# Optimization experiments

Hardware: AMD Instinct MI355X
Metric: run time of the kernel (lower is better)

Reference implementation:

```python
import jax, jax.numpy as jnp
import numpy as np

B, S, D = 1, 2048, 2048
H, KV, HD = 16, 8, 128
FF = 6144
EPS = 1e-6
THETA = 1e6
PRUNE_K = int(0.3 * S)  # tokens evicted this layer


def _rms(x, w):
    v = jnp.mean(jnp.square(x), axis=-1, keepdims=True)
    return x * jax.lax.rsqrt(v + EPS) * w


def _rope(x, cos, sin):
    # x: [B, h, S, HD]; rotate_half convention (Qwen/LLaMA style)
    x1, x2 = jnp.split(x, 2, axis=-1)
    rot = jnp.concatenate([-x2, x1], axis=-1)
    return x * cos + rot * sin


def setup_inputs() -> dict:
    key = jax.random.key(0)
    ks = jax.random.split(key, 8)
    sc = 0.02
    causal = jnp.where(jnp.tril(jnp.ones((S, S), bool)), 0.0, -1e9).astype(jnp.float32)
    return {
        "hidden_states": jax.random.normal(ks[0], (B, S, D), jnp.float32),
        "causal_mask": causal[None, None],  # [1,1,S,S]
        "positions": jnp.arange(S, dtype=jnp.int32),
        "in_ln_w": jnp.ones((D,), jnp.float32),
        "post_ln_w": jnp.ones((D,), jnp.float32),
        "q_norm_w": jnp.ones((HD,), jnp.float32),
        "k_norm_w": jnp.ones((HD,), jnp.float32),
        "Wq": jax.random.normal(ks[1], (D, H * HD), jnp.float32) * sc,
        "Wk": jax.random.normal(ks[2], (D, KV * HD), jnp.float32) * sc,
        "Wv": jax.random.normal(ks[3], (D, KV * HD), jnp.float32) * sc,
        "Wo": jax.random.normal(ks[4], (H * HD, D), jnp.float32) * sc,
        "W_gate": jax.random.normal(ks[5], (D, FF), jnp.float32) * sc,
        "W_up": jax.random.normal(ks[6], (D, FF), jnp.float32) * sc,
        "W_down": jax.random.normal(ks[7], (FF, D), jnp.float32) * sc,
    }


def reference(hidden_states, causal_mask, positions, in_ln_w, post_ln_w,
              q_norm_w, k_norm_w, Wq, Wk, Wv, Wo, W_gate, W_up, W_down):
    # Rotary tables (Qwen3 rope_theta)
    inv = 1.0 / (THETA ** (jnp.arange(0, HD, 2, dtype=jnp.float32) / HD))
    ang = positions.astype(jnp.float32)[:, None] * inv[None, :]      # [S, HD/2]
    cos = jnp.concatenate([jnp.cos(ang)] * 2, -1)[None, None]        # [1,1,S,HD]
    sin = jnp.concatenate([jnp.sin(ang)] * 2, -1)[None, None]

    # --- self attention block ---
    x = _rms(hidden_states, in_ln_w)
    q = (x @ Wq).reshape(B, S, H, HD).transpose(0, 2, 1, 3)
    k = (x @ Wk).reshape(B, S, KV, HD).transpose(0, 2, 1, 3)
    v = (x @ Wv).reshape(B, S, KV, HD).transpose(0, 2, 1, 3)
    q = _rope(_rms(q, q_norm_w), cos, sin)   # Qwen3 per-head QK-norm then RoPE
    k = _rope(_rms(k, k_norm_w), cos, sin)
    rep = H // KV
    k = jnp.repeat(k, rep, axis=1)
    v = jnp.repeat(v, rep, axis=1)
    scores = jnp.einsum('bhqd,bhkd->bhqk', q, k) / np.float32(np.sqrt(HD)) + causal_mask
    attn = jax.nn.softmax(scores, axis=-1)   # [B,H,S,S] (output_attentions=True)
    ctx = jnp.einsum('bhqk,bhkd->bhqd', attn, v)
    attn_out = ctx.transpose(0, 2, 1, 3).reshape(B, S, H * HD) @ Wo
    h = hidden_states + attn_out

    # --- MLP block (SwiGLU) ---
    y = _rms(h, post_ln_w)
    mlp = (jax.nn.silu(y @ W_gate) * (y @ W_up)) @ W_down
    out = h + mlp

    # --- importance scoring + top-k pruning (prefill: last token is index S-1) ---
    importance = jnp.sum(attn[:, :, S - 1, :], axis=(0, 1)) / (B * H)  # [S]
    importance = importance.at[S - 1].set(jnp.inf)  # never prune the last token
    _, prune_idxs = jax.lax.top_k(-importance, PRUNE_K)  # k smallest scores
    return out, attn, prune_idxs
```

## Files before the change

kernel.cpp:

```cpp
#include <hip/hip_runtime.h>
#include <math.h>

#define Sn 2048
#define Dm 2048
#define Hn 16
#define KVn 8
#define HD 128
#define FFn 6144
#define PK 614

#define BM 64
#define BN 64
#define BK 16

typedef __attribute__((ext_vector_type(8))) short short8;
typedef __attribute__((ext_vector_type(4))) float f32x4;

__device__ __forceinline__ short f2bf(float f) {
    unsigned u = __float_as_uint(f);
    u += 0x7fff + ((u >> 16) & 1);
    return (short)(u >> 16);
}

__device__ __forceinline__ void gload16(const void* g, void* l) {
    __builtin_amdgcn_global_load_lds((const __attribute__((address_space(1))) void*)g,
                                     (__attribute__((address_space(3))) void*)l, 16, 0, 0);
}

template<typename ACC, int MODE>
__global__ __launch_bounds__(256)
void gemm_k(const float* __restrict__ A, int lda, long long strideA,
            const float* __restrict__ B, int ldb, long long strideB, int bshift,
            float* __restrict__ C, int ldc, long long strideC,
            const float* __restrict__ resid,
            int M, int N, int K, float alpha, int causal)
{
    const int bx = blockIdx.x, by = blockIdx.y, bz = blockIdx.z;
    const int bm0 = by * BM, bn0 = bx * BN;
    if (MODE == 1 && causal == 1 && bn0 > bm0 + BM - 1) return;

    A += (long long)bz * strideA;
    B += (long long)(bz >> bshift) * strideB;
    C += (long long)bz * strideC;

    __shared__ float As[BK][BM + 4];
    __shared__ float Bs[BK][BN + 4];

    const int tid = threadIdx.x;
    const int tx = tid & 15, ty = tid >> 4;

    ACC acc[4][4];
    #pragma unroll
    for (int i = 0; i < 4; i++)
        #pragma unroll
        for (int j = 0; j < 4; j++) acc[i][j] = (ACC)0;

    for (int k0 = 0; k0 < K; k0 += BK) {
        {
            int c = tid & 15, r0 = tid >> 4;
            #pragma unroll
            for (int i = 0; i < 4; i++) {
                int r = r0 + 16 * i;
                As[c][r] = A[(long long)(bm0 + r) * lda + (k0 + c)];
            }
        }
        if (MODE == 1) {
            int c = tid & 15, r0 = tid >> 4;
            #pragma unroll
            for (int i = 0; i < 4; i++) {
                int r = r0 + 16 * i;
                Bs[c][r] = B[(long long)(bn0 + r) * ldb + (k0 + c)];
            }
        } else {
            int c = tid & 63, r0 = tid >> 6;
            #pragma unroll
            for (int i = 0; i < 4; i++) {
                int r = r0 + 4 * i;
                Bs[r][c] = B[(long long)(k0 + r) * ldb + (bn0 + c)];
            }
        }
        __syncthreads();
        #pragma unroll
        for (int kk = 0; kk < BK; kk++) {
            float4 av = *(const float4*)&As[kk][ty * 4];
            float4 bv = *(const float4*)&Bs[kk][tx * 4];
            float a_[4] = {av.x, av.y, av.z, av.w};
            float b_[4] = {bv.x, bv.y, bv.z, bv.w};
            #pragma unroll
            for (int i = 0; i < 4; i++)
                #pragma unroll
                for (int j = 0; j < 4; j++)
                    acc[i][j] += (ACC)a_[i] * (ACC)b_[j];
        }
        __syncthreads();
    }

    #pragma unroll
    for (int i = 0; i < 4; i++) {
        int m = bm0 + ty * 4 + i;
        #pragma unroll
        for (int j = 0; j < 4; j++) {
            int n = bn0 + tx * 4 + j;
            float val = (float)(acc[i][j] * (ACC)alpha);
            if (resid) val += resid[(long long)m * ldc + n];
            C[(long long)m * ldc + n] = val;
        }
    }
}

template<int MODE>
__global__ __launch_bounds__(256)
void mgemm_k(const short* __restrict__ A, int lda,
             const short* __restrict__ B, int ldb,
             const short* __restrict__ B2,
             float* __restrict__ Cf, short* __restrict__ Cb, int ldc,
             const float* __restrict__ resid, int K)
{
    __shared__ short As[128 * 64];
    __shared__ short Bs[128 * 64];
    __shared__ short B2s[(MODE == 1) ? 128 * 64 : 16];

    const int tid = threadIdx.x, lane = tid & 63, wv = tid >> 6;
    const int wm = wv & 1, wn = wv >> 1;
    const int l15 = lane & 15, q4 = lane >> 4;
    const int bm0 = blockIdx.y * 128, bn0 = blockIdx.x * 128;

    f32x4 acc[4][4];
    f32x4 acc2[(MODE == 1) ? 4 : 1][(MODE == 1) ? 4 : 1];
    #pragma unroll
    for (int i = 0; i < 4; i++)
        #pragma unroll
        for (int j = 0; j < 4; j++) {
            acc[i][j] = (f32x4)0.0f;
            if constexpr (MODE == 1) acc2[i][j] = (f32x4)0.0f;
        }

    for (int k0 = 0; k0 < K; k0 += 64) {
        #pragma unroll
        for (int r = 0; r < 4; r++) {
            int c = (wv * 4 + r) * 64 + lane;
            int row = c >> 3, co = (c & 7) * 8;
            gload16(A + (size_t)(bm0 + row) * lda + k0 + co, (char*)As + (size_t)c * 16);
            gload16(B + (size_t)(bn0 + row) * ldb + k0 + co, (char*)Bs + (size_t)c * 16);
            if constexpr (MODE == 1)
                gload16(B2 + (size_t)(bn0 + row) * ldb + k0 + co, (char*)B2s + (size_t)c * 16);
        }
        __syncthreads();
        #pragma unroll
        for (int kk = 0; kk < 2; kk++) {
            short8 af[4], bfr[4], b2f[4];
            #pragma unroll
            for (int i = 0; i < 4; i++)
                af[i] = *(const short8*)&As[(size_t)(wm * 64 + i * 16 + l15) * 64 + kk * 32 + q4 * 8];
            #pragma unroll
            for (int j = 0; j < 4; j++) {
                bfr[j] = *(const short8*)&Bs[(size_t)(wn * 64 + j * 16 + l15) * 64 + kk * 32 + q4 * 8];
                if constexpr (MODE == 1)
                    b2f[j] = *(const short8*)&B2s[(size_t)(wn * 64 + j * 16 + l15) * 64 + kk * 32 + q4 * 8];
            }
            #pragma unroll
            for (int i = 0; i < 4; i++)
                #pragma unroll
                for (int j = 0; j < 4; j++) {
                    acc[i][j] = __builtin_amdgcn_mfma_f32_16x16x32_bf16(af[i], bfr[j], acc[i][j], 0, 0, 0);
                    if constexpr (MODE == 1)
                        acc2[i][j] = __builtin_amdgcn_mfma_f32_16x16x32_bf16(af[i], b2f[j], acc2[i][j], 0, 0, 0);
                }
        }
        __syncthreads();
    }

    #pragma unroll
    for (int i = 0; i < 4; i++)
        #pragma unroll
        for (int j = 0; j < 4; j++)
            #pragma unroll
            for (int r = 0; r < 4; r++) {
                int m = bm0 + wm * 64 + i * 16 + q4 * 4 + r;
                int n = bn0 + wn * 64 + j * 16 + l15;
                float vv = acc[i][j][r];
                if constexpr (MODE == 0) {
                    if (resid) vv += resid[(size_t)m * ldc + n];
                    Cf[(size_t)m * ldc + n] = vv;
                } else if constexpr (MODE == 1) {
                    float u = acc2[i][j][r];
                    Cb[(size_t)m * ldc + n] = f2bf(vv / (1.0f + expf(-vv)) * u);
                } else {
                    Cb[(size_t)n * ldc + m] = f2bf(vv);
                }
            }
}

__global__ __launch_bounds__(256)
void ctx_k(const float* __restrict__ P, const short* __restrict__ Vt,
           short* __restrict__ Cb)
{
    __shared__ float Af[128 * 64];
    __shared__ short Bs[128 * 64];

    const int h = blockIdx.z;
    const float* A = P + (size_t)h * Sn * Sn;
    const short* B = Vt + (size_t)(h >> 1) * HD * Sn;

    const int tid = threadIdx.x, lane = tid & 63, wv = tid >> 6;
    const int wm = wv & 1, wn = wv >> 1;
    const int l15 = lane & 15, q4 = lane >> 4;
    const int bm0 = blockIdx.y * 128;
    const int Keff = bm0 + 128;

    f32x4 acc[4][4];
    #pragma unroll
    for (int i = 0; i < 4; i++)
        #pragma unroll
        for (int j = 0; j < 4; j++) acc[i][j] = (f32x4)0.0f;

    for (int k0 = 0; k0 < Keff; k0 += 64) {
        #pragma unroll
        for (int r = 0; r < 8; r++) {
            int c = (wv * 8 + r) * 64 + lane;
            int row = c >> 4, co = (c & 15) * 4;
            gload16(A + (size_t)(bm0 + row) * Sn + k0 + co, (char*)Af + (size_t)c * 16);
        }
        #pragma unroll
        for (int r = 0; r < 4; r++) {
            int c = (wv * 4 + r) * 64 + lane;
            int row = c >> 3, co = (c & 7) * 8;
            gload16(B + (size_t)row * Sn + k0 + co, (char*)Bs + (size_t)c * 16);
        }
        __syncthreads();
        #pragma unroll
        for (int kk = 0; kk < 2; kk++) {
            short8 af[4], bfr[4];
            #pragma unroll
            for (int i = 0; i < 4; i++) {
                const float* ap = &Af[(size_t)(wm * 64 + i * 16 + l15) * 64 + kk * 32 + q4 * 8];
                f32x4 a0 = *(const f32x4*)ap;
                f32x4 a1 = *(const f32x4*)(ap + 4);
                short8 t;
                t[0] = f2bf(a0[0]); t[1] = f2bf(a0[1]); t[2] = f2bf(a0[2]); t[3] = f2bf(a0[3]);
                t[4] = f2bf(a1[0]); t[5] = f2bf(a1[1]); t[6] = f2bf(a1[2]); t[7] = f2bf(a1[3]);
                af[i] = t;
            }
            #pragma unroll
            for (int j = 0; j < 4; j++)
                bfr[j] = *(const short8*)&Bs[(size_t)(wn * 64 + j * 16 + l15) * 64 + kk * 32 + q4 * 8];
            #pragma unroll
            for (int i = 0; i < 4; i++)
                #pragma unroll
                for (int j = 0; j < 4; j++)
                    acc[i][j] = __builtin_amdgcn_mfma_f32_16x16x32_bf16(af[i], bfr[j], acc[i][j], 0, 0, 0);
        }
        __syncthreads();
    }

    #pragma unroll
    for (int i = 0; i < 4; i++)
        #pragma unroll
        for (int j = 0; j < 4; j++)
            #pragma unroll
            for (int r = 0; r < 4; r++) {
                int m = bm0 + wm * 64 + i * 16 + q4 * 4 + r;
                int n = wn * 64 + j * 16 + l15;
                Cb[(size_t)m * Dm + h * HD + n] = f2bf(acc[i][j][r]);
            }
}

__global__ __launch_bounds__(256)
void castT_k(const float* __restrict__ W, int ldw, int row0, int col0,
             short* __restrict__ Wt, int ldt)
{
    __shared__ float t[64][65];
    const int tr = threadIdx.x >> 6, tc = threadIdx.x & 63;
    const int gr = blockIdx.y * 64, gc = blockIdx.x * 64;
    #pragma unroll
    for (int rr = tr; rr < 64; rr += 4)
        t[rr][tc] = W[(size_t)(row0 + gr + rr) * ldw + col0 + gc + tc];
    __syncthreads();
    #pragma unroll
    for (int cc = tr; cc < 64; cc += 4)
        Wt[(size_t)(gc + cc) * ldt + gr + tc] = f2bf(t[tc][cc]);
}

__global__ __launch_bounds__(256)
void rmsnorm_k(const float* __restrict__ in, const float* __restrict__ w,
               float* __restrict__ o, short* __restrict__ ob)
{
    const int row = blockIdx.x;
    const float* x = in + (long long)row * Dm;
    const int tid = threadIdx.x;
    double ss = 0.0;
    #pragma unroll
    for (int rb = 0; rb < 8; rb++) {
        float t = x[tid + rb * 256];
        ss += (double)t * (double)t;
    }
    #pragma unroll
    for (int off = 32; off > 0; off >>= 1) ss += __shfl_xor(ss, off, 64);
    __shared__ double sh[4];
    int lane = tid & 63, wvv = tid >> 6;
    if (lane == 0) sh[wvv] = ss;
    __syncthreads();
    double tot = sh[0] + sh[1] + sh[2] + sh[3];
    double scale = 1.0 / sqrt(tot / (double)Dm + (double)1e-6f);
    #pragma unroll
    for (int rb = 0; rb < 8; rb++) {
        int j = tid + rb * 256;
        float val = (float)((double)x[j] * scale * (double)w[j]);
        if (o)  o[(long long)row * Dm + j] = val;
        if (ob) ob[(long long)row * Dm + j] = f2bf(val);
    }
}

__global__ __launch_bounds__(256)
void rope_table_k(const int* __restrict__ positions,
                  double* __restrict__ ct, double* __restrict__ st)
{
    int idx = blockIdx.x * 256 + threadIdx.x;
    if (idx >= Sn * 64) return;
    int s = idx >> 6, j = idx & 63;
    float e = (float)j * (1.0f / 64.0f);
    float p32 = (float)pow(1.0e6, (double)e);
    float invf = (float)(1.0 / (double)p32);
    float ang = (float)positions[s] * invf;
    ct[idx] = cos((double)ang);
    st[idx] = sin((double)ang);
}

__global__ __launch_bounds__(128)
void qknorm_rope_k(float* __restrict__ buf, int ld, int nh,
                   const float* __restrict__ w,
                   const double* __restrict__ ct, const double* __restrict__ st)
{
    const int b = blockIdx.x;
    const int h = b % nh, s = b / nh;
    float* p = buf + (long long)s * ld + h * HD;
    const int d = threadIdx.x;
    const int pd = (d < 64) ? d + 64 : d - 64;
    float a = p[d];
    float pv = p[pd];
    double ss = (double)a * (double)a;
    #pragma unroll
    for (int o = 32; o > 0; o >>= 1) ss += __shfl_xor(ss, o, 64);
    __shared__ double sh[2];
    if ((d & 63) == 0) sh[d >> 6] = ss;
    __syncthreads();
    double tot = sh[0] + sh[1];
    double scale = 1.0 / sqrt(tot / (double)HD + (double)1e-6f);
    double xn = (double)a * scale * (double)w[d];
    double pn = (double)pv * scale * (double)w[pd];
    double rot = (d < 64) ? -pn : pn;
    int j = d & 63;
    double c = ct[s * 64 + j], snv = st[s * 64 + j];
    p[d] = (float)(xn * c + rot * snv);
}

__global__ __launch_bounds__(256)
void qlast_proj_k(const float* __restrict__ x, const float* __restrict__ Wq,
                  double* __restrict__ qlast)
{
    __shared__ double part[4][64];
    const int kq = threadIdx.x >> 6, nn = threadIdx.x & 63;
    const int n = blockIdx.x * 64 + nn;
    const float* xr = x + (size_t)(Sn - 1) * Dm;
    double acc = 0.0;
    for (int k = kq; k < Dm; k += 4)
        acc += (double)xr[k] * (double)Wq[(size_t)k * Dm + n];
    part[kq][nn] = acc;
    __syncthreads();
    if (kq == 0)
        qlast[n] = part[0][nn] + part[1][nn] + part[2][nn] + part[3][nn];
}

__global__ __launch_bounds__(128)
void qlast_nr_k(const double* __restrict__ qlast, const float* __restrict__ w,
                const double* __restrict__ ct, const double* __restrict__ st,
                double* __restrict__ qhat)
{
    const int h = blockIdx.x, d = threadIdx.x;
    const int pd = (d < 64) ? d + 64 : d - 64;
    double a = qlast[h * HD + d];
    double pv = qlast[h * HD + pd];
    double ss = a * a;
    #pragma unroll
    for (int o = 32; o > 0; o >>= 1) ss += __shfl_xor(ss, o, 64);
    __shared__ double sh[2];
    if ((d & 63) == 0) sh[d >> 6] = ss;
    __syncthreads();
    double tot = sh[0] + sh[1];
    double scale = 1.0 / sqrt(tot / (double)HD + (double)1e-6f);
    double xn = a * scale * (double)w[d];
    double pn = pv * scale * (double)w[pd];
    double rot = (d < 64) ? -pn : pn;
    int j = d & 63;
    double c = ct[(Sn - 1) * 64 + j], snv = st[(Sn - 1) * 64 + j];
    qhat[h * HD + d] = xn * c + rot * snv;
}

__global__ __launch_bounds__(256)
void imp_scores_k(const double* __restrict__ qhat, const float* __restrict__ khat,
                  double* __restrict__ phead)
{
    const int h = blockIdx.x, kv = h >> 1;
    __shared__ double sc[Sn];
    __shared__ double qv[HD];
    __shared__ double sh[4];
    const int tid = threadIdx.x;
    if (tid < HD) qv[tid] = qhat[h * HD + tid];
    __syncthreads();
    const double s128 = (double)sqrtf(128.0f);
    for (int j = tid; j < Sn; j += 256) {
        const float* kr = khat + (long long)j * (KVn * HD) + kv * HD;
        double acc = 0.0;
        #pragma unroll 8
        for (int dd = 0; dd < HD; dd++) acc += qv[dd] * (double)kr[dd];
        sc[j] = acc / s128;
    }
    __syncthreads();
    double m = -1.0e300;
    for (int j = tid; j < Sn; j += 256) m = fmax(m, sc[j]);
    #pragma unroll
    for (int o = 32; o > 0; o >>= 1) m = fmax(m, __shfl_xor(m, o, 64));
    if ((tid & 63) == 0) sh[tid >> 6] = m;
    __syncthreads();
    m = fmax(fmax(sh[0], sh[1]), fmax(sh[2], sh[3]));
    __syncthreads();
    double ssum = 0.0;
    for (int j = tid; j < Sn; j += 256) {
        double e = exp(sc[j] - m);
        sc[j] = e;
        ssum += e;
    }
    #pragma unroll
    for (int o = 32; o > 0; o >>= 1) ssum += __shfl_xor(ssum, o, 64);
    if ((tid & 63) == 0) sh[tid >> 6] = ssum;
    __syncthreads();
    double tot = sh[0] + sh[1] + sh[2] + sh[3];
    for (int j = tid; j < Sn; j += 256)
        phead[(long long)h * Sn + j] = sc[j] / tot;
}

__global__ __launch_bounds__(1024)
void imp_sort_k(const double* __restrict__ phead, float* __restrict__ out_idx)
{
    __shared__ unsigned long long keys[Sn];
    const int tid = threadIdx.x;
    for (int j = tid; j < Sn; j += 1024) {
        double s = 0.0;
        #pragma unroll
        for (int h = 0; h < Hn; h++) s += phead[(long long)h * Sn + j];
        float imp = (float)(s * (1.0 / 16.0));
        if (j == Sn - 1) imp = __builtin_inff();
        unsigned u = __float_as_uint(imp);
        keys[j] = ((unsigned long long)u << 32) | (unsigned)j;
    }
    __syncthreads();
    for (int k = 2; k <= Sn; k <<= 1) {
        for (int jj = k >> 1; jj > 0; jj >>= 1) {
            for (int i = tid; i < Sn; i += 1024) {
                int p = i ^ jj;
                if (p > i) {
                    unsigned long long a = keys[i], b = keys[p];
                    bool up = ((i & k) == 0);
                    if ((a > b) == up) { keys[i] = b; keys[p] = a; }
                }
            }
            __syncthreads();
        }
    }
    if (tid < PK)
        out_idx[tid] = (float)(unsigned)(keys[tid] & 0xffffffffULL);
}

__global__ __launch_bounds__(256)
void softmax_k(float* __restrict__ attn)
{
    const long long row = blockIdx.x;
    const int i = (int)(row & (Sn - 1));
    float* p = attn + row * Sn;
    const int tid = threadIdx.x;
    float v[8];
    float mx = -1e30f;
    #pragma unroll
    for (int rb = 0; rb < 8; rb++) {
        int j = tid + rb * 256;
        if (j <= i) { v[rb] = p[j]; mx = fmaxf(mx, v[rb]); }
        else        v[rb] = 0.0f;
    }
    #pragma unroll
    for (int o = 32; o > 0; o >>= 1) mx = fmaxf(mx, __shfl_xor(mx, o, 64));
    __shared__ float shm[4], shs[4];
    int lane = tid & 63, wvv = tid >> 6;
    if (lane == 0) shm[wvv] = mx;
    __syncthreads();
    mx = fmaxf(fmaxf(shm[0], shm[1]), fmaxf(shm[2], shm[3]));
    float sum = 0.0f;
    #pragma unroll
    for (int rb = 0; rb < 8; rb++) {
        int j = tid + rb * 256;
        if (j <= i) { v[rb] = expf(v[rb] - mx); sum += v[rb]; }
        else        v[rb] = 0.0f;
    }
    #pragma unroll
    for (int o = 32; o > 0; o >>= 1) sum += __shfl_xor(sum, o, 64);
    if (lane == 0) shs[wvv] = sum;
    __syncthreads();
    sum = shs[0] + shs[1] + shs[2] + shs[3];
    float inv = 1.0f / sum;
    #pragma unroll
    for (int rb = 0; rb < 8; rb++) {
        int j = tid + rb * 256;
        p[j] = v[rb] * inv;
    }
}

extern "C" void kernel_launch(void* const* d_in, const int* in_sizes, int n_in,
                              void* d_out, int out_size, void* d_ws, size_t ws_size,
                              hipStream_t stream)
{
    const float* hidden    = (const float*)d_in[0];
    const int*   positions = (const int*)d_in[2];
    const float* in_ln_w   = (const float*)d_in[3];
    const float* post_ln_w = (const float*)d_in[4];
    const float* q_norm_w  = (const float*)d_in[5];
    const float* k_norm_w  = (const float*)d_in[6];
    const float* Wq = (const float*)d_in[7];
    const float* Wk = (const float*)d_in[8];
    const float* Wv = (const float*)d_in[9];
    const float* Wo = (const float*)d_in[10];
    const float* Wg = (const float*)d_in[11];
    const float* Wu = (const float*)d_in[12];
    const float* Wd = (const float*)d_in[13];

    float* outp   = (float*)d_out;
    float* attn   = outp + (size_t)Sn * Dm;
    float* idxout = attn + (size_t)Hn * Sn * Sn;

    char* wsb = (char*)d_ws;
    const size_t MB = 1024 * 1024;
    float* x     = (float*)(wsb + 0 * MB);
    float* q     = (float*)(wsb + 16 * MB);
    float* kbuf  = (float*)(wsb + 32 * MB);
    short* x_b   = (short*)(wsb + 40 * MB);
    short* WvT   = (short*)(wsb + 48 * MB);
    short* vt    = (short*)(wsb + 52 * MB);
    short* WoT   = (short*)(wsb + 56 * MB);
    short* ctx_b = (short*)(wsb + 64 * MB);
    float* hbuf  = (float*)(wsb + 72 * MB);
    short* y_b   = (short*)(wsb + 88 * MB);
    double* qlast = (double*)(wsb + 96 * MB);
    double* qhat  = qlast + 2048;
    double* phead = qhat + 2048;
    double* ct    = phead + (size_t)Hn * Sn;
    double* st    = ct + (size_t)Sn * 64;
    short* WgT = (short*)(wsb + 0 * MB);
    short* WuT = (short*)(wsb + 12 * MB);
    short* hg  = (short*)(wsb + 24 * MB);
    short* WdT = (short*)(wsb + 36 * MB);

    const float inv_s128 = 1.0f / sqrtf(128.0f);

    rmsnorm_k<<<Sn, 256, 0, stream>>>(hidden, in_ln_w, x, x_b);
    rope_table_k<<<(Sn * 64) / 256, 256, 0, stream>>>(positions, ct, st);
    castT_k<<<dim3(1024 / 64, 2048 / 64), 256, 0, stream>>>(Wv, KVn * HD, 0, 0, WvT, Dm);
    gemm_k<float, 0><<<dim3(Dm / BN, Sn / BM, 1), 256, 0, stream>>>(
        x, Dm, 0, Wq, Dm, 0, 0, q, Dm, 0, nullptr, Sn, Dm, Dm, 1.0f, 0);
    gemm_k<float, 0><<<dim3((KVn * HD) / BN, Sn / BM, 1), 256, 0, stream>>>(
        x, Dm, 0, Wk, KVn * HD, 0, 0, kbuf, KVn * HD, 0, nullptr, Sn, KVn * HD, Dm, 1.0f, 0);
    mgemm_k<2><<<dim3((KVn * HD) / 128, Sn / 128), 256, 0, stream>>>(
        x_b, Dm, WvT, Dm, nullptr, nullptr, vt, Sn, nullptr, Dm);
    qlast_proj_k<<<Dm / 64, 256, 0, stream>>>(x, Wq, qlast);
    qknorm_rope_k<<<Sn * Hn, 128, 0, stream>>>(q, Dm, Hn, q_norm_w, ct, st);
    qknorm_rope_k<<<Sn * KVn, 128, 0, stream>>>(kbuf, KVn * HD, KVn, k_norm_w, ct, st);
    qlast_nr_k<<<Hn, 128, 0, stream>>>(qlast, q_norm_w, ct, st, qhat);
    gemm_k<float, 1><<<dim3(Sn / BN, Sn / BM, Hn), 256, 0, stream>>>(
        q, Dm, HD, kbuf, KVn * HD, HD, 1,
        attn, Sn, (long long)Sn * Sn, nullptr, Sn, Sn, HD, inv_s128, 1);
    softmax_k<<<Hn * Sn, 256, 0, stream>>>(attn);
    imp_scores_k<<<Hn, 256, 0, stream>>>(qhat, kbuf, phead);
    imp_sort_k<<<1, 1024, 0, stream>>>(phead, idxout);
    castT_k<<<dim3(2048 / 64, 2048 / 64), 256, 0, stream>>>(Wo, Dm, 0, 0, WoT, Dm);
    ctx_k<<<dim3(1, Sn / 128, Hn), 256, 0, stream>>>(attn, vt, ctx_b);
    mgemm_k<0><<<dim3(Dm / 128, Sn / 128), 256, 0, stream>>>(
        ctx_b, Dm, WoT, Dm, nullptr, hbuf, nullptr, Dm, hidden, Dm);
    rmsnorm_k<<<Sn, 256, 0, stream>>>(hbuf, post_ln_w, nullptr, y_b);
    for (int ch = 0; ch < 2; ch++) {
        castT_k<<<dim3(3072 / 64, 2048 / 64), 256, 0, stream>>>(Wg, FFn, 0, ch * 3072, WgT, Dm);
        castT_k<<<dim3(3072 / 64, 2048 / 64), 256, 0, stream>>>(Wu, FFn, 0, ch * 3072, WuT, Dm);
        mgemm_k<1><<<dim3(3072 / 128, Sn / 128), 256, 0, stream>>>(
            y_b, Dm, WgT, Dm, WuT, nullptr, hg, 3072, nullptr, Dm);
        castT_k<<<dim3(2048 / 64, 3072 / 64), 256, 0, stream>>>(Wd, Dm, ch * 3072, 0, WdT, 3072);
        mgemm_k<0><<<dim3(Dm / 128, Sn / 128), 256, 0, stream>>>(
            hg, 3072, WdT, 3072, nullptr, outp, nullptr, Dm,
            (ch == 0) ? hbuf : outp, 3072);
    }
    (void)in_sizes; (void)n_in; (void)out_size; (void)ws_size;
}
```

Baseline: 2.058 ms.

## Use split-bf16 MFMA GEMMs for Q projection and QK scores, rework softmax and ctx

Replaces the fp32 gemm_k for the Q projection and the causal QK^T score computation with a new msplit_k kernel. It splits fp32 operands into bf16 hi/lo pairs and runs three bf16 MFMA passes (hi*hi, hi*lo, lo*hi) to approximate fp32 accuracy on matrix cores. Softmax now handles one row per wavefront with vectorized loads, no block-level syncs, and only touches the causal prefix. ctx_k moves to 64-row tiles, doubling the block count. The trade is extra split kernels, extra workspace traffic, and a reduced-precision product that may shift results slightly.

```diff
diff --git a/kernel.cpp b/kernel.cpp
--- a/kernel.cpp
+++ b/kernel.cpp
@@ -14,12 +14,17 @@
 #define BK 16
 
 typedef __attribute__((ext_vector_type(8))) short short8;
+typedef __attribute__((ext_vector_type(4))) short s16x4;
 typedef __attribute__((ext_vector_type(4))) float f32x4;
 
 __device__ __forceinline__ short f2bf(float f) {
     unsigned u = __float_as_uint(f);
     u += 0x7fff + ((u >> 16) & 1);
     return (short)(u >> 16);
+}
+
+__device__ __forceinline__ float bf2f(short h) {
+    return __uint_as_float((unsigned)(unsigned short)h << 16);
 }
 
 __device__ __forceinline__ void gload16(const void* g, void* l) {
@@ -192,10 +197,85 @@
 }
 
 __global__ __launch_bounds__(256)
+void msplit_k(const short* __restrict__ Ah, const short* __restrict__ Al,
+              int lda, long long strideA,
+              const short* __restrict__ Bh, const short* __restrict__ Bl,
+              int ldb, long long strideB, int bshift,
+              float* __restrict__ C, int ldc, long long strideC,
+              float alpha, int K, int causal)
+{
+    const int bm0 = blockIdx.y * 128, bn0 = blockIdx.x * 128;
+    if (causal && bn0 > bm0 + 127) return;
+    const int bz = blockIdx.z;
+    const long long aoff = (long long)bz * strideA;
+    const long long boff = (long long)(bz >> bshift) * strideB;
+    Ah += aoff; Al += aoff;
+    Bh += boff; Bl += boff;
+    C += (long long)bz * strideC;
+
+    __shared__ short As[128 * 64];
+    __shared__ short Bs[128 * 64];
+
+    const int tid = threadIdx.x, lane = tid & 63, wv = tid >> 6;
+    const int wm = wv & 1, wn = wv >> 1;
+    const int l15 = lane & 15, q4 = lane >> 4;
+
+    f32x4 acc[4][4];
+    #pragma unroll
+    for (int i = 0; i < 4; i++)
+        #pragma unroll
+        for (int j = 0; j < 4; j++) acc[i][j] = (f32x4)0.0f;
+
+    const int K3 = 3 * K;
+    for (int k0 = 0; k0 < K3; k0 += 64) {
+        const short* Ap = Ah;
+        const short* Bp = Bh;
+        int kb = k0;
+        if (k0 >= 2 * K)      { Ap = Al; kb = k0 - 2 * K; }
+        else if (k0 >= K)     { Bp = Bl; kb = k0 - K; }
+        #pragma unroll
+        for (int r = 0; r < 4; r++) {
+            int c = (wv * 4 + r) * 64 + lane;
+            int row = c >> 3, co = (c & 7) * 8;
+            gload16(Ap + (size_t)(bm0 + row) * lda + kb + co, (char*)As + (size_t)c * 16);
+            gload16(Bp + (size_t)(bn0 + row) * ldb + kb + co, (char*)Bs + (size_t)c * 16);
+        }
+        __syncthreads();
+        #pragma unroll
+        for (int kk = 0; kk < 2; kk++) {
+            short8 af[4], bfr[4];
+            #pragma unroll
+            for (int i = 0; i < 4; i++)
+                af[i] = *(const short8*)&As[(size_t)(wm * 64 + i * 16 + l15) * 64 + kk * 32 + q4 * 8];
+            #pragma unroll
+            for (int j = 0; j < 4; j++)
+                bfr[j] = *(const short8*)&Bs[(size_t)(wn * 64 + j * 16 + l15) * 64 + kk * 32 + q4 * 8];
+            #pragma unroll
+            for (int i = 0; i < 4; i++)
+                #pragma unroll
+                for (int j = 0; j < 4; j++)
+                    acc[i][j] = __builtin_amdgcn_mfma_f32_16x16x32_bf16(af[i], bfr[j], acc[i][j], 0, 0, 0);
+        }
+        __syncthreads();
+    }
+
+    #pragma unroll
+    for (int i = 0; i < 4; i++)
+        #pragma unroll
+        for (int j = 0; j < 4; j++)
+            #pragma unroll
+            for (int r = 0; r < 4; r++) {
+                int m = bm0 + wm * 64 + i * 16 + q4 * 4 + r;
+                int n = bn0 + wn * 64 + j * 16 + l15;
+                C[(size_t)m * ldc + n] = acc[i][j][r] * alpha;
+            }
+}
+
+__global__ __launch_bounds__(256)
 void ctx_k(const float* __restrict__ P, const short* __restrict__ Vt,
            short* __restrict__ Cb)
 {
-    __shared__ float Af[128 * 64];
+    __shared__ float Af[64 * 64];
     __shared__ short Bs[128 * 64];
 
     const int h = blockIdx.z;
@@ -205,19 +285,19 @@
     const int tid = threadIdx.x, lane = tid & 63, wv = tid >> 6;
     const int wm = wv & 1, wn = wv >> 1;
     const int l15 = lane & 15, q4 = lane >> 4;
-    const int bm0 = blockIdx.y * 128;
-    const int Keff = bm0 + 128;
-
-    f32x4 acc[4][4];
-    #pragma unroll
-    for (int i = 0; i < 4; i++)
+    const int bm0 = blockIdx.y * 64;
+    const int Keff = bm0 + 64;
+
+    f32x4 acc[2][4];
+    #pragma unroll
+    for (int i = 0; i < 2; i++)
         #pragma unroll
         for (int j = 0; j < 4; j++) acc[i][j] = (f32x4)0.0f;
 
     for (int k0 = 0; k0 < Keff; k0 += 64) {
         #pragma unroll
-        for (int r = 0; r < 8; r++) {
-            int c = (wv * 8 + r) * 64 + lane;
+        for (int r = 0; r < 4; r++) {
+            int c = (wv * 4 + r) * 64 + lane;
             int row = c >> 4, co = (c & 15) * 4;
             gload16(A + (size_t)(bm0 + row) * Sn + k0 + co, (char*)Af + (size_t)c * 16);
         }
@@ -230,10 +310,10 @@
         __syncthreads();
         #pragma unroll
         for (int kk = 0; kk < 2; kk++) {
-            short8 af[4], bfr[4];
-            #pragma unroll
-            for (int i = 0; i < 4; i++) {
-                const float* ap = &Af[(size_t)(wm * 64 + i * 16 + l15) * 64 + kk * 32 + q4 * 8];
+            short8 af[2], bfr[4];
+            #pragma unroll
+            for (int i = 0; i < 2; i++) {
+                const float* ap = &Af[(size_t)(wm * 32 + i * 16 + l15) * 64 + kk * 32 + q4 * 8];
                 f32x4 a0 = *(const f32x4*)ap;
                 f32x4 a1 = *(const f32x4*)(ap + 4);
                 short8 t;
@@ -245,7 +325,7 @@
             for (int j = 0; j < 4; j++)
                 bfr[j] = *(const short8*)&Bs[(size_t)(wn * 64 + j * 16 + l15) * 64 + kk * 32 + q4 * 8];
             #pragma unroll
-            for (int i = 0; i < 4; i++)
+            for (int i = 0; i < 2; i++)
                 #pragma unroll
                 for (int j = 0; j < 4; j++)
                     acc[i][j] = __builtin_amdgcn_mfma_f32_16x16x32_bf16(af[i], bfr[j], acc[i][j], 0, 0, 0);
@@ -254,12 +334,12 @@
     }
 
     #pragma unroll
-    for (int i = 0; i < 4; i++)
+    for (int i = 0; i < 2; i++)
         #pragma unroll
         for (int j = 0; j < 4; j++)
             #pragma unroll
             for (int r = 0; r < 4; r++) {
-                int m = bm0 + wm * 64 + i * 16 + q4 * 4 + r;
+                int m = bm0 + wm * 32 + i * 16 + q4 * 4 + r;
                 int n = wn * 64 + j * 16 + l15;
                 Cb[(size_t)m * Dm + h * HD + n] = f2bf(acc[i][j][r]);
             }
@@ -267,7 +347,7 @@
 
 __global__ __launch_bounds__(256)
 void castT_k(const float* __restrict__ W, int ldw, int row0, int col0,
-             short* __restrict__ Wt, int ldt)
+             short* __restrict__ Wt, short* __restrict__ Wlo, int ldt)
 {
     __shared__ float t[64][65];
     const int tr = threadIdx.x >> 6, tc = threadIdx.x & 63;
@@ -277,13 +357,37 @@
         t[rr][tc] = W[(size_t)(row0 + gr + rr) * ldw + col0 + gc + tc];
     __syncthreads();
     #pragma unroll
-    for (int cc = tr; cc < 64; cc += 4)
-        Wt[(size_t)(gc + cc) * ldt + gr + tc] = f2bf(t[tc][cc]);
+    for (int cc = tr; cc < 64; cc += 4) {
+        float v = t[tc][cc];
+        short h = f2bf(v);
+        size_t off = (size_t)(gc + cc) * ldt + gr + tc;
+        Wt[off] = h;
+        if (Wlo) Wlo[off] = f2bf(v - bf2f(h));
+    }
+}
+
+__global__ __launch_bounds__(256)
+void split_k(const float* __restrict__ in, short* __restrict__ hi,
+             short* __restrict__ lo, int n4)
+{
+    int i = blockIdx.x * 256 + threadIdx.x;
+    if (i >= n4) return;
+    f32x4 v = *(const f32x4*)(in + (size_t)i * 4);
+    s16x4 h, l;
+    #pragma unroll
+    for (int j = 0; j < 4; j++) {
+        short hh = f2bf(v[j]);
+        h[j] = hh;
+        l[j] = f2bf(v[j] - bf2f(hh));
+    }
+    *(s16x4*)(hi + (size_t)i * 4) = h;
+    *(s16x4*)(lo + (size_t)i * 4) = l;
 }
 
 __global__ __launch_bounds__(256)
 void rmsnorm_k(const float* __restrict__ in, const float* __restrict__ w,
-               float* __restrict__ o, short* __restrict__ ob)
+               float* __restrict__ o, short* __restrict__ ob,
+               short* __restrict__ obl)
 {
     const int row = blockIdx.x;
     const float* x = in + (long long)row * Dm;
@@ -307,7 +411,11 @@
         int j = tid + rb * 256;
         float val = (float)((double)x[j] * scale * (double)w[j]);
         if (o)  o[(long long)row * Dm + j] = val;
-        if (ob) ob[(long long)row * Dm + j] = f2bf(val);
+        if (ob) {
+            short h = f2bf(val);
+            ob[(long long)row * Dm + j] = h;
+            if (obl) obl[(long long)row * Dm + j] = f2bf(val - bf2f(h));
+        }
     }
 }
 
@@ -474,42 +582,64 @@
 __global__ __launch_bounds__(256)
 void softmax_k(float* __restrict__ attn)
 {
-    const long long row = blockIdx.x;
+    const int wv = threadIdx.x >> 6, lane = threadIdx.x & 63;
+    const long long row = (long long)blockIdx.x * 4 + wv;
     const int i = (int)(row & (Sn - 1));
     float* p = attn + row * Sn;
-    const int tid = threadIdx.x;
-    float v[8];
+    const int E = ((i >> 7) + 1) << 7;
+    const int nit = (E + 255) >> 8;
+
+    f32x4 v[8];
     float mx = -1e30f;
     #pragma unroll
-    for (int rb = 0; rb < 8; rb++) {
-        int j = tid + rb * 256;
-        if (j <= i) { v[rb] = p[j]; mx = fmaxf(mx, v[rb]); }
-        else        v[rb] = 0.0f;
+    for (int it = 0; it < 8; it++) {
+        if (it < nit) {
+            int j4 = (it * 64 + lane) * 4;
+            f32x4 t;
+            if (j4 < E) {
+                t = *(const f32x4*)(p + j4);
+                #pragma unroll
+                for (int c = 0; c < 4; c++) {
+                    if (j4 + c > i) t[c] = -1e30f;
+                    mx = fmaxf(mx, t[c]);
+                }
+            } else {
+                t = (f32x4)(-1e30f);
+            }
+            v[it] = t;
+        }
     }
     #pragma unroll
     for (int o = 32; o > 0; o >>= 1) mx = fmaxf(mx, __shfl_xor(mx, o, 64));
-    __shared__ float shm[4], shs[4];
-    int lane = tid & 63, wvv = tid >> 6;
-    if (lane == 0) shm[wvv] = mx;
-    __syncthreads();
-    mx = fmaxf(fmaxf(shm[0], shm[1]), fmaxf(shm[2], shm[3]));
+
     float sum = 0.0f;
     #pragma unroll
-    for (int rb = 0; rb < 8; rb++) {
-        int j = tid + rb * 256;
-        if (j <= i) { v[rb] = expf(v[rb] - mx); sum += v[rb]; }
-        else        v[rb] = 0.0f;
+    for (int it = 0; it < 8; it++) {
+        if (it < nit) {
+            f32x4 t = v[it];
+            #pragma unroll
+            for (int c = 0; c < 4; c++) {
+                float e = (t[c] > -1e29f) ? expf(t[c] - mx) : 0.0f;
+                t[c] = e;
+                sum += e;
+            }
+            v[it] = t;
+        }
     }
     #pragma unroll
     for (int o = 32; o > 0; o >>= 1) sum += __shfl_xor(sum, o, 64);
-    if (lane == 0) shs[wvv] = sum;
-    __syncthreads();
-    sum = shs[0] + shs[1] + shs[2] + shs[3];
     float inv = 1.0f / sum;
-    #pragma unroll
-    for (int rb = 0; rb < 8; rb++) {
-        int j = tid + rb * 256;
-        p[j] = v[rb] * inv;
+
+    #pragma unroll
+    for (int it = 0; it < 8; it++) {
+        if (it < nit) {
+            int j4 = (it * 64 + lane) * 4;
+            if (j4 < E) {
+                f32x4 t = v[it];
+                t[0] *= inv; t[1] *= inv; t[2] *= inv; t[3] *= inv;
+                *(f32x4*)(p + j4) = t;
+            }
+        }
     }
 }
 
@@ -552,6 +682,12 @@
     double* phead = qhat + 2048;
     double* ct    = phead + (size_t)Hn * Sn;
     double* st    = ct + (size_t)Sn * 64;
+    short* x_lo = (short*)(wsb + 99 * MB);
+    short* WqTh = (short*)(wsb + 107 * MB);
+    short* WqTl = (short*)(wsb + 115 * MB);
+    short* k_hi = (short*)(wsb + 123 * MB);
+    short* k_lo = (short*)(wsb + 127 * MB);
+    short* q_hi = WqTh; short* q_lo = WqTl;
     short* WgT = (short*)(wsb + 0 * MB);
     short* WuT = (short*)(wsb + 12 * MB);
     short* hg  = (short*)(wsb + 24 * MB);
@@ -559,11 +695,12 @@
 
     const float inv_s128 = 1.0f / sqrtf(128.0f);
 
-    rmsnorm_k<<<Sn, 256, 0, stream>>>(hidden, in_ln_w, x, x_b);
+    rmsnorm_k<<<Sn, 256, 0, stream>>>(hidden, in_ln_w, x, x_b, x_lo);
     rope_table_k<<<(Sn * 64) / 256, 256, 0, stream>>>(positions, ct, st);
-    castT_k<<<dim3(1024 / 64, 2048 / 64), 256, 0, stream>>>(Wv, KVn * HD, 0, 0, WvT, Dm);
-    gemm_k<float, 0><<<dim3(Dm / BN, Sn / BM, 1), 256, 0, stream>>>(
-        x, Dm, 0, Wq, Dm, 0, 0, q, Dm, 0, nullptr, Sn, Dm, Dm, 1.0f, 0);
+    castT_k<<<dim3(1024 / 64, 2048 / 64), 256, 0, stream>>>(Wv, KVn * HD, 0, 0, WvT, nullptr, Dm);
+    castT_k<<<dim3(2048 / 64, 2048 / 64), 256, 0, stream>>>(Wq, Dm, 0, 0, WqTh, WqTl, Dm);
+    msplit_k<<<dim3(Dm / 128, Sn / 128, 1), 256, 0, stream>>>(
+        x_b, x_lo, Dm, 0, WqTh, WqTl, Dm, 0, 0, q, Dm, 0, 1.0f, Dm, 0);
     gemm_k<float, 0><<<dim3((KVn * HD) / BN, Sn / BM, 1), 256, 0, stream>>>(
         x, Dm, 0, Wk, KVn * HD, 0, 0, kbuf, KVn * HD, 0, nullptr, Sn, KVn * HD, Dm, 1.0f, 0);
     mgemm_k<2><<<dim3((KVn * HD) / 128, Sn / 128), 256, 0, stream>>>(
@@ -572,23 +709,25 @@
     qknorm_rope_k<<<Sn * Hn, 128, 0, stream>>>(q, Dm, Hn, q_norm_w, ct, st);
     qknorm_rope_k<<<Sn * KVn, 128, 0, stream>>>(kbuf, KVn * HD, KVn, k_norm_w, ct, st);
     qlast_nr_k<<<Hn, 128, 0, stream>>>(qlast, q_norm_w, ct, st, qhat);
-    gemm_k<float, 1><<<dim3(Sn / BN, Sn / BM, Hn), 256, 0, stream>>>(
-        q, Dm, HD, kbuf, KVn * HD, HD, 1,
-        attn, Sn, (long long)Sn * Sn, nullptr, Sn, Sn, HD, inv_s128, 1);
-    softmax_k<<<Hn * Sn, 256, 0, stream>>>(attn);
+    split_k<<<(Sn * Dm / 4) / 256, 256, 0, stream>>>(q, q_hi, q_lo, Sn * Dm / 4);
+    split_k<<<(Sn * KVn * HD / 4) / 256, 256, 0, stream>>>(kbuf, k_hi, k_lo, Sn * KVn * HD / 4);
+    msplit_k<<<dim3(Sn / 128, Sn / 128, Hn), 256, 0, stream>>>(
+        q_hi, q_lo, Dm, HD, k_hi, k_lo, KVn * HD, HD, 1,
+        attn, Sn, (long long)Sn * Sn, inv_s128, HD, 1);
+    softmax_k<<<(Hn * Sn) / 4, 256, 0, stream>>>(attn);
     imp_scores_k<<<Hn, 256, 0, stream>>>(qhat, kbuf, phead);
     imp_sort_k<<<1, 1024, 0, stream>>>(phead, idxout);
-    castT_k<<<dim3(2048 / 64, 2048 / 64), 256, 0, stream>>>(Wo, Dm, 0, 0, WoT, Dm);
-    ctx_k<<<dim3(1, Sn / 128, Hn), 256, 0, stream>>>(attn, vt, ctx_b);
+    castT_k<<<dim3(2048 / 64, 2048 / 64), 256, 0, stream>>>(Wo, Dm, 0, 0, WoT, nullptr, Dm);
+    ctx_k<<<dim3(1, Sn / 64, Hn), 256, 0, stream>>>(attn, vt, ctx_b);
     mgemm_k<0><<<dim3(Dm / 128, Sn / 128), 256, 0, stream>>>(
         ctx_b, Dm, WoT, Dm, nullptr, hbuf, nullptr, Dm, hidden, Dm);
-    rmsnorm_k<<<Sn, 256, 0, stream>>>(hbuf, post_ln_w, nullptr, y_b);
+    rmsnorm_k<<<Sn, 256, 0, stream>>>(hbuf, post_ln_w, nullptr, y_b, nullptr);
     for (int ch = 0; ch < 2; ch++) {
-        castT_k<<<dim3(3072 / 64, 2048 / 64), 256, 0, stream>>>(Wg, FFn, 0, ch * 3072, WgT, Dm);
-        castT_k<<<dim3(3072 / 64, 2048 / 64), 256, 0, stream>>>(Wu, FFn, 0, ch * 3072, WuT, Dm);
+        castT_k<<<dim3(3072 / 64, 2048 / 64), 256, 0, stream>>>(Wg, FFn, 0, ch * 3072, WgT, nullptr, Dm);
+        castT_k<<<dim3(3072 / 64, 2048 / 64), 256, 0, stream>>>(Wu, FFn, 0, ch * 3072, WuT, nullptr, Dm);
         mgemm_k<1><<<dim3(3072 / 128, Sn / 128), 256, 0, stream>>>(
             y_b, Dm, WgT, Dm, WuT, nullptr, hg, 3072, nullptr, Dm);
-        castT_k<<<dim3(2048 / 64, 3072 / 64), 256, 0, stream>>>(Wd, Dm, ch * 3072, 0, WdT, 3072);
+        castT_k<<<dim3(2048 / 64, 3072 / 64), 256, 0, stream>>>(Wd, Dm, ch * 3072, 0, WdT, nullptr, 3072);
         mgemm_k<0><<<dim3(Dm / 128, Sn / 128), 256, 0, stream>>>(
             hg, 3072, WdT, 3072, nullptr, outp, nullptr, Dm,
             (ch == 0) ? hbuf : outp, 3072);
```

Measured after the change: 1.775 ms, median of 2. 13.7% less time.
